# Kernel optimization log

Measured on AMD Instinct MI355X. Metric: run time of the kernel, lower is better.

The kernel has to match this reference:

```python
import jax, jax.numpy as jnp
import numpy as np

B, S, D = 4, 2048, 2048
H, G, HD = 16, 4, 128  # num_heads, kv groups, head_dim
THETA = 10000.0


def setup_inputs() -> dict:
    key = jax.random.key(0)
    ks = jax.random.split(key, 5)
    sc_in = 1.0 / np.sqrt(D)
    sc_out = 1.0 / np.sqrt(H * HD)
    return {
        "x": jax.random.normal(ks[0], (B, S, D), jnp.float32),
        "Wq": jax.random.normal(ks[1], (D, H, HD), jnp.float32) * sc_in,
        "bq": jnp.zeros((H, HD), jnp.float32),
        "Wk": jax.random.normal(ks[2], (D, G, HD), jnp.float32) * sc_in,
        "bk": jnp.zeros((G, HD), jnp.float32),
        "Wv": jax.random.normal(ks[3], (D, G, HD), jnp.float32) * sc_in,
        "bv": jnp.zeros((G, HD), jnp.float32),
        "Wo": jax.random.normal(ks[4], (H, HD, D), jnp.float32) * sc_out,
        "bo": jnp.zeros((D,), jnp.float32),
    }


def _rope(q, k):
    # q: [B,S,H,HD], k: [B,S,G,HD]; LLaMA-style rotate-half RoPE
    half = HD // 2
    inv_freq = 1.0 / (THETA ** (jnp.arange(0, HD, 2, dtype=jnp.float32) / HD))  # [half]
    ang = jnp.arange(S, dtype=jnp.float32)[:, None] * inv_freq  # [S, half]
    cos = jnp.cos(ang)[None, :, None, :]  # [1,S,1,half]
    sin = jnp.sin(ang)[None, :, None, :]

    def rot(t):
        t1, t2 = t[..., :half], t[..., half:]
        return jnp.concatenate([t1 * cos - t2 * sin, t2 * cos + t1 * sin], axis=-1)

    return rot(q), rot(k)


def reference(x, Wq, bq, Wk, bk, Wv, bv, Wo, bo):
    q = jnp.einsum("bsd,dhk->bshk", x, Wq) + bq  # [B,S,H,HD]
    k = jnp.einsum("bsd,dgk->bsgk", x, Wk) + bk  # [B,S,G,HD]
    v = jnp.einsum("bsd,dgk->bsgk", x, Wv) + bv
    q, k = _rope(q, k)
    # replicate_for_multi_query: repeat kv heads to num_heads
    k = jnp.repeat(k, H // G, axis=-2)  # [B,S,H,HD]
    v = jnp.repeat(v, H // G, axis=-2)
    scale = 1.0 / jnp.sqrt(jnp.asarray(HD, q.dtype))
    scores = jnp.einsum("bqhd,bkhd->bhqk", q * scale, k)  # [B,H,S,S]
    causal = jnp.tril(jnp.ones((S, S), bool))
    scores = jnp.where(causal[None, None], scores, jnp.finfo(scores.dtype).min)
    w = jax.nn.softmax(scores, axis=-1)
    attn = jnp.einsum("bhqk,bkhd->bqhd", w, v)  # [B,S,H,HD]
    return jnp.einsum("bqhd,hdo->bqo", attn, Wo) + bo
```

## Files before the change

kernel.cpp:

```cpp
#include <hip/hip_runtime.h>
#include <hip/hip_bf16.h>
#include <math.h>

#define B_  4
#define S_  2048
#define D_  2048
#define H_  16
#define G_  4
#define HD_ 128

typedef __attribute__((ext_vector_type(8))) short short8;
typedef __attribute__((ext_vector_type(4))) float floatx4;

__device__ __forceinline__ short f2bf(float f) {
    unsigned u = __float_as_uint(f);
    unsigned r = (u + 0x7fff + ((u >> 16) & 1)) >> 16;
    return (short)r;
}
__device__ __forceinline__ float b2f(short s) {
    return __uint_as_float(((unsigned)(unsigned short)s) << 16);
}
__device__ __forceinline__ unsigned pk2(float a, float b) {
    unsigned ua = (__float_as_uint(a) + 0x8000u) >> 16;
    unsigned ub = (__float_as_uint(b) + 0x8000u) & 0xffff0000u;
    return ua | ub;
}
__device__ __forceinline__ unsigned pkr(float a, float b) {
    return (unsigned)(unsigned short)f2bf(a) |
           ((unsigned)(unsigned short)f2bf(b) << 16);
}

#define GLL16(gp, lp) __builtin_amdgcn_global_load_lds( \
    (const __attribute__((address_space(1))) void*)(gp), \
    (__attribute__((address_space(3))) void*)(lp), 16, 0, 0)

__global__ void cvt_bf16_kernel(const float* __restrict__ in,
                                short* __restrict__ out, int n8)
{
    int t = blockIdx.x * 256 + threadIdx.x;
    if (t >= n8) return;
    const float4* p = (const float4*)in + (size_t)t * 2;
    float4 a = p[0], b = p[1];
    short8 r;
    r[0] = f2bf(a.x); r[1] = f2bf(a.y); r[2] = f2bf(a.z); r[3] = f2bf(a.w);
    r[4] = f2bf(b.x); r[5] = f2bf(b.y); r[6] = f2bf(b.z); r[7] = f2bf(b.w);
    ((short8*)out)[t] = r;
}

__global__ __launch_bounds__(256) void tr_bf16_kernel(
    const float* __restrict__ in, short* __restrict__ out, int K, int N)
{
    __shared__ float T[32][33];
    int n0 = blockIdx.x * 32, k0 = blockIdx.y * 32;
    int tx = threadIdx.x & 31, ty = threadIdx.x >> 5;
#pragma unroll
    for (int i = 0; i < 4; ++i)
        T[ty + i * 8][tx] = in[(size_t)(k0 + ty + i * 8) * N + n0 + tx];
    __syncthreads();
#pragma unroll
    for (int i = 0; i < 4; ++i)
        out[(size_t)(n0 + ty + i * 8) * K + k0 + tx] = f2bf(T[tx][ty + i * 8]);
}

__global__ __launch_bounds__(512, 2) void gemm256_8ph(
    const short* __restrict__ A, const short* __restrict__ Bt,
    int M, int N, int K, int qkvmode,
    const float* __restrict__ b0, const float* __restrict__ b1,
    const float* __restrict__ b2, float* __restrict__ Cf,
    short* __restrict__ qo, short* __restrict__ ko, short* __restrict__ vo)
{
    __shared__ short L[65536];
    const int tid = threadIdx.x;
    const int w = tid >> 6, lane = tid & 63, l15 = lane & 15, quad = lane >> 4;
    const int wm = w >> 2, wn = w & 3;
    const int n0 = blockIdx.x * 256, m0 = blockIdx.y * 256;
    const int NT = K >> 6;

    const int srow = tid >> 2;
    const int gch8 = ((tid & 3) ^ (srow & 3)) * 8;
    const int csw8 = (quad ^ (l15 & 3)) * 8;

    floatx4 acc[8][4];
#pragma unroll
    for (int f = 0; f < 8; ++f)
#pragma unroll
        for (int g = 0; g < 4; ++g) acc[f][g] = (floatx4){0.f, 0.f, 0.f, 0.f};

    const short* Ab = A  + (size_t)(m0 + srow) * K + gch8;
    const short* Bb = Bt + (size_t)(n0 + srow) * K + gch8;
    const size_t rj = (size_t)128 * K;

#define STGA(tt, KH, DB) do { \
    const short* s_ = Ab + (size_t)(tt) * 64 + (KH) * 32; \
    short* d_ = L + (DB) * 32768 + (KH) * 8192 + tid * 8; \
    GLL16(s_, d_); GLL16(s_ + rj, d_ + 4096); } while (0)
#define STGB(tt, KH, DB) do { \
    const short* s_ = Bb + (size_t)(tt) * 64 + (KH) * 32; \
    short* d_ = L + (DB) * 32768 + 16384 + (KH) * 8192 + tid * 8; \
    GLL16(s_, d_); GLL16(s_ + rj, d_ + 4096); } while (0)

    STGA(0, 0, 0); STGB(0, 0, 0); STGA(0, 1, 0); STGB(0, 1, 0);
    asm volatile("s_waitcnt vmcnt(4)" ::: "memory");
    asm volatile("s_barrier" ::: "memory");

#define PH(KS, FH, STAGE_STMT) do { \
    short8 afr[4], bfr[4]; \
    _Pragma("unroll") \
    for (int i = 0; i < 4; ++i) \
        afr[i] = *(const short8*)(ab + (KS) * 8192 + \
                 (wm * 128 + ((FH) * 4 + i) * 16 + l15) * 32 + csw8); \
    _Pragma("unroll") \
    for (int g = 0; g < 4; ++g) \
        bfr[g] = *(const short8*)(bb + (KS) * 8192 + \
                 (wn * 64 + g * 16 + l15) * 32 + csw8); \
    STAGE_STMT; \
    __builtin_amdgcn_s_setprio(1); \
    _Pragma("unroll") \
    for (int i = 0; i < 4; ++i) { \
        acc[(FH)*4+i][0] = __builtin_amdgcn_mfma_f32_16x16x32_bf16(afr[i], bfr[0], acc[(FH)*4+i][0], 0, 0, 0); \
        acc[(FH)*4+i][1] = __builtin_amdgcn_mfma_f32_16x16x32_bf16(afr[i], bfr[1], acc[(FH)*4+i][1], 0, 0, 0); \
        acc[(FH)*4+i][2] = __builtin_amdgcn_mfma_f32_16x16x32_bf16(afr[i], bfr[2], acc[(FH)*4+i][2], 0, 0, 0); \
        acc[(FH)*4+i][3] = __builtin_amdgcn_mfma_f32_16x16x32_bf16(afr[i], bfr[3], acc[(FH)*4+i][3], 0, 0, 0); \
    } \
    __builtin_amdgcn_s_setprio(0); } while (0)

#define PHW \
    asm volatile("s_waitcnt vmcnt(4)" ::: "memory"); \
    asm volatile("s_barrier" ::: "memory");

    for (int t = 0; t < NT - 1; ++t) {
        const int cur = t & 1, nxt = cur ^ 1;
        const short* ab = L + cur * 32768;
        const short* bb = ab + 16384;
        PH(0, 0, STGA(t + 1, 0, nxt)); PHW;
        PH(0, 1, STGB(t + 1, 0, nxt)); PHW;
        PH(1, 0, STGA(t + 1, 1, nxt)); PHW;
        PH(1, 1, STGB(t + 1, 1, nxt)); PHW;
    }
    asm volatile("s_waitcnt vmcnt(0)" ::: "memory");
    asm volatile("s_barrier" ::: "memory");
    {
        const int cur = (NT - 1) & 1;
        const short* ab = L + cur * 32768;
        const short* bb = ab + 16384;
        PH(0, 0, (void)0); PH(0, 1, (void)0);
        PH(1, 0, (void)0); PH(1, 1, (void)0);
    }

    if (!qkvmode) {
#pragma unroll
        for (int f = 0; f < 8; ++f) {
            int grow = m0 + wm * 128 + f * 16 + quad * 4;
#pragma unroll
            for (int g = 0; g < 4; ++g) {
                int gcol = n0 + wn * 64 + g * 16 + l15;
                float bvv = b0[gcol];
                floatx4 v = acc[f][g];
#pragma unroll
                for (int r = 0; r < 4; ++r)
                    Cf[(size_t)(grow + r) * N + gcol] = v[r] + bvv;
            }
        }
    } else {
#pragma unroll
        for (int g = 0; g < 4; ++g) {
            int gcol = n0 + wn * 64 + g * 16 + l15;
            float bvv = (gcol < 2048) ? b0[gcol]
                      : (gcol < 2560) ? b1[gcol - 2048] : b2[gcol - 2560];
#pragma unroll
            for (int f = 0; f < 8; ++f) {
                int grow = m0 + wm * 128 + f * 16 + quad * 4;
                floatx4 v = acc[f][g];
                if (n0 < 2048) {
#pragma unroll
                    for (int r = 0; r < 4; ++r)
                        qo[(size_t)(grow + r) * 2048 + gcol] = f2bf(v[r] + bvv);
                } else if (n0 < 2560) {
                    int c = gcol - 2048;
#pragma unroll
                    for (int r = 0; r < 4; ++r)
                        ko[(size_t)(grow + r) * 512 + c] = f2bf(v[r] + bvv);
                } else {
                    int c = gcol - 2560, gg = c >> 7, dv = c & 127;
                    int bb2 = grow >> 11, s = grow & 2047;
                    uint2 pk;
                    pk.x = pkr(v[0] + bvv, v[1] + bvv);
                    pk.y = pkr(v[2] + bvv, v[3] + bvv);
                    *(uint2*)&vo[(((size_t)bb2 * G_ + gg) * HD_ + dv) * S_ + s] = pk;
                }
            }
        }
    }
#undef PH
#undef PHW
#undef STGA
#undef STGB
}

__global__ void rope_bf16_kernel(short* __restrict__ p, int nh, float scale,
                                 int total)
{
    int gid = blockIdx.x * 256 + threadIdx.x;
    if (gid >= total) return;
    int i = gid & 63;
    int rest = gid >> 6;
    int head = rest % nh;
    int rest2 = rest / nh;
    int s = rest2 & (S_ - 1);
    int b = rest2 >> 11;
    size_t base = (((size_t)b * S_ + s) * nh + head) * HD_;
    float inv = __expf((float)i * -0.14391156509f);
    float ang = (float)s * inv;
    float sn, cs;
    sincosf(ang, &sn, &cs);
    float t1 = b2f(p[base + i]), t2 = b2f(p[base + 64 + i]);
    p[base + i]      = f2bf((t1 * cs - t2 * sn) * scale);
    p[base + 64 + i] = f2bf((t2 * cs + t1 * sn) * scale);
}

#define PPITCH 72

__global__ __launch_bounds__(256) void attn_mfma2(
    short* __restrict__ qb, const short* __restrict__ kb,
    const short* __restrict__ vt)
{
    __shared__ short Ks[64 * 128];
    __shared__ short Vs[128 * 64];
    __shared__ short Ps[4][32 * PPITCH];

    const int tid = threadIdx.x;
    const int w = tid >> 6, lane = tid & 63, l15 = lane & 15, quad = lane >> 4;
    const int id = (int)blockIdx.x;
    const int j = id >> 6, grp = j >> 2, pos = j & 3;
    const int qi = (grp == 0) ? (15 - pos)
                 : (grp == 1) ? pos
                 : (grp == 2) ? (11 - pos) : (4 + pos);
    const int q0 = qi * 128;
    const int bh = id & 63, b = bh >> 4, h = bh & 15, g = h >> 2;

    const short* qp = qb + ((((size_t)b * S_) + q0 + w * 32 + l15) * H_ + h) * HD_
                      + quad * 8;
    short8 qf[2][4];
#pragma unroll
    for (int qs = 0; qs < 2; ++qs)
#pragma unroll
        for (int c = 0; c < 4; ++c)
            qf[qs][c] = *(const short8*)(qp + qs * 16 * (H_ * HD_) + c * 32);

    floatx4 ot[2][8];
#pragma unroll
    for (int qs = 0; qs < 2; ++qs)
#pragma unroll
        for (int s = 0; s < 8; ++s) ot[qs][s] = (floatx4){0.f, 0.f, 0.f, 0.f};
    float m_i[2] = {-1e30f, -1e30f}, l_i[2] = {0.f, 0.f};

    const int kkey = tid >> 4, kch = tid & 15;
    const int ksrc = kch ^ (kkey & 7);
    const short* kgb = kb + (((size_t)b * S_) * G_ + g) * HD_ + ksrc * 8;
    const int vdv = tid >> 3, vch = tid & 7;
    const int vsrc = vch ^ (vdv & 7);
    const short* vgb = vt + (((size_t)(b * G_ + g)) * HD_ + vdv) * (size_t)S_
                       + vsrc * 8;
    const int sw = l15 & 7;
    short* pw = Ps[w];

    const int nkt = 2 * (qi + 1);
    for (int kt = 0; kt < nkt; ++kt) {
        __syncthreads();
        const short* kg = kgb + (size_t)(kt * 64) * (G_ * HD_);
        const short* vg = vgb + kt * 64;
#pragma unroll
        for (int i = 0; i < 4; ++i)
            GLL16(kg + (size_t)(kkey + 16 * i) * (G_ * HD_),
                  Ks + (w * 64 + 256 * i) * 8);
#pragma unroll
        for (int i = 0; i < 4; ++i)
            GLL16(vg + (size_t)(32 * i) * S_, Vs + (w * 64 + 256 * i) * 8);
        __syncthreads();

        floatx4 sa[2][4];
#pragma unroll
        for (int qs = 0; qs < 2; ++qs)
#pragma unroll
            for (int ks = 0; ks < 4; ++ks) sa[qs][ks] = (floatx4){0.f, 0.f, 0.f, 0.f};
#pragma unroll
        for (int c = 0; c < 4; ++c)
#pragma unroll
            for (int ks = 0; ks < 4; ++ks) {
                short8 kf = *(const short8*)(Ks +
                    ((l15 + 16 * ks) * 16 + ((c * 4 + quad) ^ sw)) * 8);
                sa[0][ks] = __builtin_amdgcn_mfma_f32_16x16x32_bf16(
                    kf, qf[0][c], sa[0][ks], 0, 0, 0);
                sa[1][ks] = __builtin_amdgcn_mfma_f32_16x16x32_bf16(
                    kf, qf[1][c], sa[1][ks], 0, 0, 0);
            }

        const int kbase = kt * 64;
#pragma unroll
        for (int qs = 0; qs < 2; ++qs) {
            const int qrow = q0 + w * 32 + qs * 16 + l15;
            if (kbase + 63 > q0 + w * 32 + qs * 16) {
#pragma unroll
                for (int ks = 0; ks < 4; ++ks)
#pragma unroll
                    for (int r = 0; r < 4; ++r)
                        if (kbase + ks * 16 + quad * 4 + r > qrow)
                            sa[qs][ks][r] = -1e30f;
            }
            float mx = -1e30f;
#pragma unroll
            for (int ks = 0; ks < 4; ++ks)
#pragma unroll
                for (int r = 0; r < 4; ++r) mx = fmaxf(mx, sa[qs][ks][r]);
            mx = fmaxf(mx, __shfl_xor(mx, 16));
            mx = fmaxf(mx, __shfl_xor(mx, 32));
            float mo = m_i[qs];
            if (!__all(mx - mo <= 11.5f)) {
                float mn = fmaxf(mo, mx);
                float al = exp2f(mo - mn);
                m_i[qs] = mn;
                l_i[qs] *= al;
#pragma unroll
                for (int s = 0; s < 8; ++s) {
                    floatx4 o = ot[qs][s];
                    o[0] *= al; o[1] *= al; o[2] *= al; o[3] *= al;
                    ot[qs][s] = o;
                }
                mo = mn;
            }
            float s0 = 0.f, s1 = 0.f, s2 = 0.f, s3 = 0.f;
#pragma unroll
            for (int ks = 0; ks < 4; ++ks) {
                float p0 = exp2f(sa[qs][ks][0] - mo);
                float p1 = exp2f(sa[qs][ks][1] - mo);
                float p2 = exp2f(sa[qs][ks][2] - mo);
                float p3 = exp2f(sa[qs][ks][3] - mo);
                sa[qs][ks][0] = p0; sa[qs][ks][1] = p1;
                sa[qs][ks][2] = p2; sa[qs][ks][3] = p3;
                s0 += p0; s1 += p1; s2 += p2; s3 += p3;
            }
            float sum = (s0 + s1) + (s2 + s3);
            sum += __shfl_xor(sum, 16);
            sum += __shfl_xor(sum, 32);
            l_i[qs] += sum;
            short* pr = pw + (qs * 16 + l15) * PPITCH;
#pragma unroll
            for (int ks = 0; ks < 4; ++ks) {
                uint2 pkv;
                pkv.x = pk2(sa[qs][ks][0], sa[qs][ks][1]);
                pkv.y = pk2(sa[qs][ks][2], sa[qs][ks][3]);
                *(uint2*)(pr + ks * 16 + quad * 4) = pkv;
            }
        }

#pragma unroll
        for (int kc = 0; kc < 2; ++kc) {
            short8 pf0 = *(const short8*)(pw + l15 * PPITCH + kc * 32 + quad * 8);
            short8 pf1 = *(const short8*)(pw + (16 + l15) * PPITCH + kc * 32 + quad * 8);
#pragma unroll
            for (int s = 0; s < 8; ++s) {
                short8 vf = *(const short8*)(Vs +
                    ((l15 + 16 * s) * 8 + ((kc * 4 + quad) ^ sw)) * 8);
                ot[0][s] = __builtin_amdgcn_mfma_f32_16x16x32_bf16(
                    vf, pf0, ot[0][s], 0, 0, 0);
                ot[1][s] = __builtin_amdgcn_mfma_f32_16x16x32_bf16(
                    vf, pf1, ot[1][s], 0, 0, 0);
            }
        }
    }

#pragma unroll
    for (int qs = 0; qs < 2; ++qs) {
        float inv = 1.f / l_i[qs];
        size_t base = ((((size_t)b * S_) + q0 + w * 32 + qs * 16 + l15) * H_ + h)
                      * HD_;
#pragma unroll
        for (int s = 0; s < 8; ++s) {
            uint2 pkv;
            pkv.x = pkr(ot[qs][s][0] * inv, ot[qs][s][1] * inv);
            pkv.y = pkr(ot[qs][s][2] * inv, ot[qs][s][3] * inv);
            *(uint2*)&qb[base + s * 16 + quad * 4] = pkv;
        }
    }
}

extern "C" void kernel_launch(void* const* d_in, const int* in_sizes, int n_in,
                              void* d_out, int out_size, void* d_ws, size_t ws_size,
                              hipStream_t stream)
{
    const float* x  = (const float*)d_in[0];
    const float* Wq = (const float*)d_in[1];
    const float* bq = (const float*)d_in[2];
    const float* Wk = (const float*)d_in[3];
    const float* bk = (const float*)d_in[4];
    const float* Wv = (const float*)d_in[5];
    const float* bv = (const float*)d_in[6];
    const float* Wo = (const float*)d_in[7];
    const float* bo = (const float*)d_in[8];
    float* out = (float*)d_out;

    short* xb  = (short*)d_ws;
    short* Wt  = xb + 16777216;
    short* qb8 = Wt + 6291456;
    short* kb8 = qb8 + 16777216;
    short* vt8 = kb8 + 4194304;

    const int M = B_ * S_;
    dim3 blk(256);

    cvt_bf16_kernel<<<8192, blk, 0, stream>>>(x, xb, 16777216 / 8);
    tr_bf16_kernel<<<dim3(64, 64), blk, 0, stream>>>(Wq, Wt, 2048, 2048);
    tr_bf16_kernel<<<dim3(16, 64), blk, 0, stream>>>(Wk, Wt + (size_t)2048 * 2048, 2048, 512);
    tr_bf16_kernel<<<dim3(16, 64), blk, 0, stream>>>(Wv, Wt + (size_t)2560 * 2048, 2048, 512);

    gemm256_8ph<<<dim3(12, 32), dim3(512), 0, stream>>>(
        xb, Wt, M, 3072, 2048, 1, bq, bk, bv, nullptr, qb8, kb8, vt8);

    tr_bf16_kernel<<<dim3(64, 64), blk, 0, stream>>>(Wo, Wt, 2048, 2048);

    const float qscale = 0.12751744417f;
    rope_bf16_kernel<<<32768, blk, 0, stream>>>(qb8, H_, qscale, M * H_ * 64);
    rope_bf16_kernel<<<8192,  blk, 0, stream>>>(kb8, G_, 1.0f,   M * G_ * 64);

    attn_mfma2<<<dim3(1024), blk, 0, stream>>>(qb8, kb8, vt8);

    gemm256_8ph<<<dim3(8, 32), dim3(512), 0, stream>>>(
        qb8, Wt, M, 2048, 2048, 0, bo, nullptr, nullptr, out,
        nullptr, nullptr, nullptr);
}
```

Baseline: 591.9 us.

## Prefetch next K/V tile into registers during attention compute, add MFMA priority

Replaces the per-iteration direct global-to-LDS loads, which sat between two barriers, with register prefetch. The next K/V tile is loaded into registers while the current tile's QK and PV MFMAs run, then written to LDS after a barrier. The MFMA sections are also wrapped in s_setprio raises. This is meant to hide global memory latency behind compute. The cost is extra VGPR pressure, which could lower occupancy, and an added LDS write pass plus barrier each iteration.

```diff
diff --git a/kernel.cpp b/kernel.cpp
--- a/kernel.cpp
+++ b/kernel.cpp
@@ -265,24 +265,41 @@
     short* pw = Ps[w];
 
     const int nkt = 2 * (qi + 1);
+
+    short8 kr[4], vr[4];
+#pragma unroll
+    for (int i = 0; i < 4; ++i)
+        kr[i] = *(const short8*)(kgb + (size_t)(kkey + 16 * i) * (G_ * HD_));
+#pragma unroll
+    for (int i = 0; i < 4; ++i)
+        vr[i] = *(const short8*)(vgb + (size_t)(32 * i) * S_);
+#pragma unroll
+    for (int i = 0; i < 4; ++i) {
+        *(short8*)(Ks + (256 * i + tid) * 8) = kr[i];
+        *(short8*)(Vs + (256 * i + tid) * 8) = vr[i];
+    }
+    asm volatile("s_waitcnt lgkmcnt(0)" ::: "memory");
+    __builtin_amdgcn_s_barrier();
+    asm volatile("" ::: "memory");
+
     for (int kt = 0; kt < nkt; ++kt) {
-        __syncthreads();
-        const short* kg = kgb + (size_t)(kt * 64) * (G_ * HD_);
-        const short* vg = vgb + kt * 64;
-#pragma unroll
-        for (int i = 0; i < 4; ++i)
-            GLL16(kg + (size_t)(kkey + 16 * i) * (G_ * HD_),
-                  Ks + (w * 64 + 256 * i) * 8);
-#pragma unroll
-        for (int i = 0; i < 4; ++i)
-            GLL16(vg + (size_t)(32 * i) * S_, Vs + (w * 64 + 256 * i) * 8);
-        __syncthreads();
+        if (kt + 1 < nkt) {
+            const short* kg1 = kgb + (size_t)((kt + 1) * 64) * (G_ * HD_);
+            const short* vg1 = vgb + (kt + 1) * 64;
+#pragma unroll
+            for (int i = 0; i < 4; ++i)
+                kr[i] = *(const short8*)(kg1 + (size_t)(kkey + 16 * i) * (G_ * HD_));
+#pragma unroll
+            for (int i = 0; i < 4; ++i)
+                vr[i] = *(const short8*)(vg1 + (size_t)(32 * i) * S_);
+        }
 
         floatx4 sa[2][4];
 #pragma unroll
         for (int qs = 0; qs < 2; ++qs)
 #pragma unroll
             for (int ks = 0; ks < 4; ++ks) sa[qs][ks] = (floatx4){0.f, 0.f, 0.f, 0.f};
+        __builtin_amdgcn_s_setprio(1);
 #pragma unroll
         for (int c = 0; c < 4; ++c)
 #pragma unroll
@@ -294,6 +311,7 @@
                 sa[1][ks] = __builtin_amdgcn_mfma_f32_16x16x32_bf16(
                     kf, qf[1][c], sa[1][ks], 0, 0, 0);
             }
+        __builtin_amdgcn_s_setprio(0);
 
         const int kbase = kt * 64;
 #pragma unroll
@@ -357,6 +375,7 @@
         for (int kc = 0; kc < 2; ++kc) {
             short8 pf0 = *(const short8*)(pw + l15 * PPITCH + kc * 32 + quad * 8);
             short8 pf1 = *(const short8*)(pw + (16 + l15) * PPITCH + kc * 32 + quad * 8);
+            __builtin_amdgcn_s_setprio(1);
 #pragma unroll
             for (int s = 0; s < 8; ++s) {
                 short8 vf = *(const short8*)(Vs +
@@ -366,7 +385,22 @@
                 ot[1][s] = __builtin_amdgcn_mfma_f32_16x16x32_bf16(
                     vf, pf1, ot[1][s], 0, 0, 0);
             }
-        }
+            __builtin_amdgcn_s_setprio(0);
+        }
+
+        asm volatile("s_waitcnt lgkmcnt(0)" ::: "memory");
+        __builtin_amdgcn_s_barrier();
+        asm volatile("" ::: "memory");
+        if (kt + 1 < nkt) {
+#pragma unroll
+            for (int i = 0; i < 4; ++i) {
+                *(short8*)(Ks + (256 * i + tid) * 8) = kr[i];
+                *(short8*)(Vs + (256 * i + tid) * 8) = vr[i];
+            }
+        }
+        asm volatile("s_waitcnt lgkmcnt(0)" ::: "memory");
+        __builtin_amdgcn_s_barrier();
+        asm volatile("" ::: "memory");
     }
 
 #pragma unroll
```

New measurement: 588.4 us. Within noise of the previous version (-0.6%).
